# Performance work log

Measured on AMD Instinct MI355X. Metric: run time of the kernel, lower is better.

The kernel has to match this reference:

```python
import jax, jax.numpy as jnp
import numpy as np

DIM = 64; HEADS = 4; HD = DIM // HEADS; TOPK = 40; RS = 2  # region_size = max(4//t_patch,1)
B = 16; T = 2048; NR = T // RS
EPS = 1e-5
SCALE = DIM ** -0.5  # qk_scale=None -> self.dim**-0.5 (as in source, NOT head_dim)


def conv1d(x, w, pad, groups=1):
    return jax.lax.conv_general_dilated(x, w, (1,), [(pad, pad)],
        dimension_numbers=('NCH', 'OIH', 'NCH'), feature_group_count=groups)


def bn(x, g, b):
    # eval-mode BatchNorm1d with fresh running stats (mean=0, var=1)
    s = g * np.float32(1.0 / np.sqrt(1.0 + EPS))
    return x * s[None, :, None] + b[None, :, None]


def _blocks(t):
    # (B, C, T) -> (B, H, NR, RS, HD)
    return t.reshape(B, HEADS, HD, NR, RS).transpose(0, 1, 3, 4, 2)


def forward(x, n1_g, n1_b, wq, bnq_g, bnq_b, wk, bnk_g, bnk_b, wv,
            lepe_w, lepe_b, out_w, out_b, n2_g, n2_b,
            fc1_w, bn1_g, bn1_b, fr, fi, frb, fib, fc2_w, bn2_g, bn2_b):
    # ---------- Time_bra: top-k region routing attention ----------
    xn = bn(x, n1_g, n1_b)
    q = bn(conv1d(xn, wq, 1), bnq_g, bnq_b)
    k = bn(conv1d(xn, wk, 1), bnk_g, bnk_b)
    v = conv1d(xn, wv, 0)
    # region pooling on detached q/k (avg_pool1d, T divisible by RS)
    qd = jax.lax.stop_gradient(q); kd = jax.lax.stop_gradient(k)
    q_r = qd.reshape(B, DIM, NR, RS).mean(-1)
    k_r = kd.reshape(B, DIM, NR, RS).mean(-1)
    a_r = jnp.einsum('bcr,bcs->brs', q_r, k_r)          # (B, NR, NR) region affinity
    idx = jax.lax.top_k(a_r, TOPK)[1]                   # (B, NR, TOPK), shared across heads
    qb = _blocks(q); kb = _blocks(k); vb = _blocks(v)   # (B, H, NR, RS, HD)
    ie = idx[:, None, :, :, None, None]                 # (B, 1, NR, TOPK, 1, 1)
    kg = jnp.take_along_axis(kb[:, :, None], ie, axis=3).reshape(B, HEADS, NR, TOPK * RS, HD)
    vg = jnp.take_along_axis(vb[:, :, None], ie, axis=3).reshape(B, HEADS, NR, TOPK * RS, HD)
    logits = jnp.einsum('bhrqd,bhrkd->bhrqk', qb, kg) * jnp.float32(SCALE)
    attn = jax.nn.softmax(logits, axis=-1)
    o = jnp.einsum('bhrqk,bhrkd->bhrqd', attn, vg)      # (B, H, NR, RS, HD)
    o = o.transpose(0, 1, 4, 2, 3).reshape(B, DIM, T)
    o = o + conv1d(v, lepe_w, 1, groups=DIM) + lepe_b[None, :, None]  # lepe (depthwise)
    o = conv1d(o, out_w, 0) + out_b[None, :, None]
    x = x + o
    # ---------- Frequencydomain_FFN ----------
    yn = bn(x, n2_g, n2_b)
    h = jax.nn.relu(bn(conv1d(yn, fc1_w, 0), bn1_g, bn1_b))  # (B, 2C, T)
    h = h.transpose(0, 2, 1)                                  # (B, T, 2C)
    f = jnp.fft.fft(h, axis=1, norm='ortho')
    # torch.einsum('bnc,cc->bnc', x, r) contracts with diag(r) (repeated index)
    xr = jax.nn.relu(jnp.einsum('bnc,cc->bnc', f.real, fr) - jnp.einsum('bnc,cc->bnc', f.imag, fi) + frb)
    xi = jax.nn.relu(jnp.einsum('bnc,cc->bnc', f.imag, fr) + jnp.einsum('bnc,cc->bnc', f.real, fi) + fib)
    h = jnp.fft.ifft(jax.lax.complex(xr, xi), axis=1, norm='ortho').real.astype(jnp.float32)
    h = bn(conv1d(h.transpose(0, 2, 1), fc2_w, 0), bn2_g, bn2_b)
    return x + h


def setup_inputs() -> dict:
    ks = jax.random.split(jax.random.key(0), 16)
    C = DIM; C2 = 2 * DIM
    g = lambda i, shape, s: (s * jax.random.normal(ks[i], shape)).astype(jnp.float32)
    return {
        'x': jax.random.normal(ks[0], (B, C, T), dtype=jnp.float32),
        'n1_g': jnp.ones((C,), jnp.float32), 'n1_b': jnp.zeros((C,), jnp.float32),
        'wq': g(1, (C, C, 3), 0.05), 'bnq_g': jnp.ones((C,), jnp.float32), 'bnq_b': jnp.zeros((C,), jnp.float32),
        'wk': g(2, (C, C, 3), 0.05), 'bnk_g': jnp.ones((C,), jnp.float32), 'bnk_b': jnp.zeros((C,), jnp.float32),
        'wv': g(3, (C, C, 1), 0.05),
        'lepe_w': g(4, (C, 1, 3), 0.1), 'lepe_b': jnp.zeros((C,), jnp.float32),
        'out_w': g(5, (C, C, 1), 0.05), 'out_b': jnp.zeros((C,), jnp.float32),
        'n2_g': jnp.ones((C,), jnp.float32), 'n2_b': jnp.zeros((C,), jnp.float32),
        'fc1_w': g(6, (C2, C, 1), 0.05), 'bn1_g': jnp.ones((C2,), jnp.float32), 'bn1_b': jnp.zeros((C2,), jnp.float32),
        'fr': g(7, (C2, C2), 0.02), 'fi': g(8, (C2, C2), 0.02),
        'frb': g(9, (C2,), 0.02), 'fib': g(10, (C2,), 0.02),
        'fc2_w': g(11, (C, C2, 1), 0.05), 'bn2_g': jnp.ones((C,), jnp.float32), 'bn2_b': jnp.zeros((C,), jnp.float32),
    }


def reference(x, n1_g, n1_b, wq, bnq_g, bnq_b, wk, bnk_g, bnk_b, wv,
              lepe_w, lepe_b, out_w, out_b, n2_g, n2_b,
              fc1_w, bn1_g, bn1_b, fr, fi, frb, fib, fc2_w, bn2_g, bn2_b):
    return forward(x, n1_g, n1_b, wq, bnq_g, bnq_b, wk, bnk_g, bnk_b, wv,
                   lepe_w, lepe_b, out_w, out_b, n2_g, n2_b,
                   fc1_w, bn1_g, bn1_b, fr, fi, frb, fib, fc2_w, bn2_g, bn2_b)
```

## Files before the change

kernel.cpp:

```cpp
#include <hip/hip_runtime.h>
#include <hip/hip_bf16.h>

#define T 2048
#define NR 1024
#define TOPK 40

static __device__ __forceinline__ float bnscale() { return 0.9999950000374997f; }

static __device__ __forceinline__ unsigned wave_umax64(unsigned x) {
  unsigned r = x, t;
  t = (unsigned)__builtin_amdgcn_update_dpp((int)r, (int)r, 0x111, 0xf, 0xf, false); r = r > t ? r : t;
  t = (unsigned)__builtin_amdgcn_update_dpp((int)r, (int)r, 0x112, 0xf, 0xf, false); r = r > t ? r : t;
  t = (unsigned)__builtin_amdgcn_update_dpp((int)r, (int)r, 0x114, 0xf, 0xf, false); r = r > t ? r : t;
  t = (unsigned)__builtin_amdgcn_update_dpp((int)r, (int)r, 0x118, 0xf, 0xf, false); r = r > t ? r : t;
  t = (unsigned)__builtin_amdgcn_update_dpp((int)r, (int)r, 0x142, 0xf, 0xf, false); r = r > t ? r : t;
  t = (unsigned)__builtin_amdgcn_update_dpp((int)r, (int)r, 0x143, 0xf, 0xf, false); r = r > t ? r : t;
  return (unsigned)__builtin_amdgcn_readlane((int)r, 63);
}

__global__ __launch_bounds__(256) void k_qkv(
    const float* __restrict__ x, const float* __restrict__ n1_g, const float* __restrict__ n1_b,
    const float* __restrict__ wq, const float* __restrict__ bnq_g, const float* __restrict__ bnq_b,
    const float* __restrict__ wk, const float* __restrict__ bnk_g, const float* __restrict__ bnk_b,
    const float* __restrict__ wv,
    float* __restrict__ q_t, float* __restrict__ k_t, float* __restrict__ v_t,
    float* __restrict__ q_rc, float* __restrict__ k_rc)
{
  const int b = blockIdx.y;
  const int tile = blockIdx.x >> 2;
  const int oc0 = (blockIdx.x & 3) * 16;
  const int t0 = tile * 64;
  const int r0 = tile * 32;
  const int tid = threadIdx.x;
  const float INVS = bnscale();

  __shared__ float xn[64][67];
  __shared__ float ot[16][67];

  for (int i = tid; i < 64 * 66; i += 256) {
    int c = i / 66, tt = i - c * 66;
    int t = t0 + tt - 1;
    float v = (t >= 0 && t < T) ? x[(size_t)(b * 64 + c) * T + t] : 0.f;
    xn[c][tt] = v * (n1_g[c] * INVS) + n1_b[c];
  }
  __syncthreads();

  const int w = tid >> 6, lane = tid & 63;
  const int ob = oc0 + __builtin_amdgcn_readfirstlane(w) * 4;

  float accq[4], acck[4], accv[4];
#pragma unroll
  for (int j = 0; j < 4; ++j) { accq[j] = 0.f; acck[j] = 0.f; accv[j] = 0.f; }

#pragma unroll 1
  for (int c0 = 0; c0 < 64; c0 += 4) {
    float xr[4][3];
#pragma unroll
    for (int cc = 0; cc < 4; ++cc) {
      xr[cc][0] = xn[c0 + cc][lane];
      xr[cc][1] = xn[c0 + cc][lane + 1];
      xr[cc][2] = xn[c0 + cc][lane + 2];
    }
#pragma unroll
    for (int o4 = 0; o4 < 4; ++o4) {
      int o = ob + o4;
      const float* wqo = wq + o * 192 + c0 * 3;
      const float* wko = wk + o * 192 + c0 * 3;
      const float* wvo = wv + o * 64 + c0;
      float aq = accq[o4], ak = acck[o4], av = accv[o4];
#pragma unroll
      for (int cc = 0; cc < 4; ++cc) {
        aq += xr[cc][0] * wqo[cc * 3 + 0] + xr[cc][1] * wqo[cc * 3 + 1] + xr[cc][2] * wqo[cc * 3 + 2];
        ak += xr[cc][0] * wko[cc * 3 + 0] + xr[cc][1] * wko[cc * 3 + 1] + xr[cc][2] * wko[cc * 3 + 2];
        av += xr[cc][1] * wvo[cc];
      }
      accq[o4] = aq; acck[o4] = ak; accv[o4] = av;
    }
  }

#pragma unroll
  for (int o4 = 0; o4 < 4; ++o4) {
    int o = ob + o4;
    ot[o - oc0][lane] = accq[o4] * (bnq_g[o] * INVS) + bnq_b[o];
  }
  __syncthreads();
  for (int i = tid; i < 1024; i += 256) {
    int cl = i & 15, tt = i >> 4;
    q_t[((size_t)(b * T + t0 + tt)) * 64 + oc0 + cl] = ot[cl][tt];
  }
  for (int i = tid; i < 512; i += 256) {
    int rr = i & 31, cl = i >> 5;
    q_rc[((size_t)(b * 64 + oc0 + cl)) * NR + r0 + rr] = 0.5f * (ot[cl][2 * rr] + ot[cl][2 * rr + 1]);
  }
  __syncthreads();

#pragma unroll
  for (int o4 = 0; o4 < 4; ++o4) {
    int o = ob + o4;
    ot[o - oc0][lane] = acck[o4] * (bnk_g[o] * INVS) + bnk_b[o];
  }
  __syncthreads();
  for (int i = tid; i < 1024; i += 256) {
    int cl = i & 15, tt = i >> 4;
    k_t[((size_t)(b * T + t0 + tt)) * 64 + oc0 + cl] = ot[cl][tt];
  }
  for (int i = tid; i < 512; i += 256) {
    int rr = i & 31, cl = i >> 5;
    k_rc[((size_t)(b * 64 + oc0 + cl)) * NR + r0 + rr] = 0.5f * (ot[cl][2 * rr] + ot[cl][2 * rr + 1]);
  }
  __syncthreads();

#pragma unroll
  for (int o4 = 0; o4 < 4; ++o4) {
    ot[ob + o4 - oc0][lane] = accv[o4];
  }
  __syncthreads();
  for (int i = tid; i < 1024; i += 256) {
    int cl = i & 15, tt = i >> 4;
    v_t[((size_t)(b * T + t0 + tt)) * 64 + oc0 + cl] = ot[cl][tt];
  }
}

__global__ __launch_bounds__(256) void k_scores(
    const float* __restrict__ q_rc, const float* __restrict__ k_rc, int* __restrict__ sel)
{
  const int b = blockIdx.y;
  const int r0 = blockIdx.x * 16;
  const int tid = threadIdx.x;
  const int w = tid >> 6, lane = tid & 63;

  __shared__ float qsT[16][68];

  for (int i = tid; i < 1024; i += 256) {
    int rr = i & 15, c = i >> 4;
    qsT[rr][c] = q_rc[((size_t)(b * 64 + c)) * NR + r0 + rr];
  }
  __syncthreads();

  const int row0 = w * 4;

  float4 acc[4][4];
#pragma unroll
  for (int r = 0; r < 4; ++r)
#pragma unroll
    for (int j = 0; j < 4; ++j) acc[r][j] = make_float4(0.f, 0.f, 0.f, 0.f);

  const float4* kp = (const float4*)(k_rc + ((size_t)b * 64) * NR);
#pragma unroll 1
  for (int c0 = 0; c0 < 64; c0 += 4) {
    float4 qv[4];
#pragma unroll
    for (int r = 0; r < 4; ++r) qv[r] = *(const float4*)&qsT[row0 + r][c0];
#pragma unroll
    for (int cc = 0; cc < 4; ++cc) {
      const float4* kr = kp + (size_t)(c0 + cc) * 256 + lane;
      float4 k0 = kr[0], k1 = kr[64], k2 = kr[128], k3 = kr[192];
      float qf[4] = { (&qv[0].x)[cc], (&qv[1].x)[cc], (&qv[2].x)[cc], (&qv[3].x)[cc] };
#pragma unroll
      for (int r = 0; r < 4; ++r) {
        float q = qf[r];
        acc[r][0].x += q * k0.x; acc[r][0].y += q * k0.y; acc[r][0].z += q * k0.z; acc[r][0].w += q * k0.w;
        acc[r][1].x += q * k1.x; acc[r][1].y += q * k1.y; acc[r][1].z += q * k1.z; acc[r][1].w += q * k1.w;
        acc[r][2].x += q * k2.x; acc[r][2].y += q * k2.y; acc[r][2].z += q * k2.z; acc[r][2].w += q * k2.w;
        acc[r][3].x += q * k3.x; acc[r][3].y += q * k3.y; acc[r][3].z += q * k3.z; acc[r][3].w += q * k3.w;
      }
    }
  }

  unsigned pk[4][16];
#pragma unroll
  for (int r = 0; r < 4; ++r) {
#pragma unroll
    for (int j = 0; j < 4; ++j) {
      const float* av = &acc[r][j].x;
#pragma unroll
      for (int s = 0; s < 4; ++s) {
        unsigned u = __float_as_uint(av[s]);
        u ^= (unsigned)((int)u >> 31) | 0x80000000u;
        int idx = 256 * j + 4 * lane + s;
        pk[r][4 * j + s] = (u & 0xFFFFFC00u) | (unsigned)(1023 - idx);
      }
    }
#pragma unroll
    for (int k = 2; k <= 16; k <<= 1) {
#pragma unroll
      for (int j = k >> 1; j > 0; j >>= 1) {
#pragma unroll
        for (int i = 0; i < 16; ++i) {
          int l = i ^ j;
          if (l > i) {
            unsigned hi = pk[r][i] > pk[r][l] ? pk[r][i] : pk[r][l];
            unsigned lo = pk[r][i] > pk[r][l] ? pk[r][l] : pk[r][i];
            bool dir = ((i & k) == 0);
            pk[r][i] = dir ? hi : lo;
            pk[r][l] = dir ? lo : hi;
          }
        }
      }
    }
  }

  int res[4] = {0, 0, 0, 0};
#pragma unroll 1
  for (int it = 0; it < TOPK; ++it) {
#pragma unroll
    for (int r = 0; r < 4; ++r) {
      unsigned bv = wave_umax64(pk[r][0]);
      if (lane == it) res[r] = 1023 - (int)(bv & 1023u);
      bool won = (pk[r][0] == bv);
#pragma unroll
      for (int s = 0; s < 15; ++s) pk[r][s] = won ? pk[r][s + 1] : pk[r][s];
      pk[r][15] = won ? 0u : pk[r][15];
    }
  }

  if (lane < TOPK) {
#pragma unroll
    for (int r = 0; r < 4; ++r)
      sel[((size_t)(b * NR + r0 + row0 + r)) * TOPK + lane] = res[r];
  }
}

__global__ __launch_bounds__(256) void k_attn(
    const float* __restrict__ q_t, const float* __restrict__ k_t, const float* __restrict__ v_t,
    const int* __restrict__ sel, const float* __restrict__ lepe_w, const float* __restrict__ lepe_b,
    float* __restrict__ o_t)
{
  const int b = blockIdx.y;
  const int r = blockIdx.x;
  const int tid = threadIdx.x;

  __shared__ __align__(16) float kg[80][68];
  __shared__ __align__(16) float qb[2][64];
  __shared__ int   toff[80];
  __shared__ __align__(16) float lg[4][2][84];
  __shared__ float vl[4][64];

  float (*part)[2][64] = (float (*)[2][64])&kg[0][0];

  if (tid < 40) {
    int s = sel[((size_t)(b * NR + r)) * TOPK + tid];
    toff[2 * tid]     = s * 512;
    toff[2 * tid + 1] = s * 512 + 256;
  }
  if (tid >= 128 && tid < 256) {
    int i = tid - 128;
    int s = i >> 6, c = i & 63;
    qb[s][c] = q_t[((size_t)(b * T + r * 2 + s)) * 64 + c];
  }
  {
    int idx = tid >> 6, c = tid & 63;
    int t = 2 * r - 1 + idx;
    vl[idx][c] = (t >= 0 && t < T) ? v_t[((size_t)(b * T + t)) * 64 + c] : 0.f;
  }
  __syncthreads();

  {
    const char* kbase = (const char*)(k_t + (size_t)b * T * 64);
    for (int i = tid; i < 80 * 16; i += 256) {
      int row = i >> 4, c4 = i & 15;
      float4 kv = *(const float4*)(kbase + toff[row] + c4 * 16);
      *(float4*)&kg[row][c4 * 4] = kv;
    }
  }
  __syncthreads();

  const int h = tid >> 6, lane = tid & 63;

  {
    float4 q0[4], q1[4];
#pragma unroll
    for (int j = 0; j < 4; ++j) {
      q0[j] = *(const float4*)&qb[0][h * 16 + j * 4];
      q1[j] = *(const float4*)&qb[1][h * 16 + j * 4];
    }
    for (int col = lane; col < 80; col += 64) {
      float a0 = 0.f, a1 = 0.f;
#pragma unroll
      for (int j = 0; j < 4; ++j) {
        float4 kv = *(const float4*)&kg[col][h * 16 + j * 4];
        a0 += q0[j].x * kv.x + q0[j].y * kv.y + q0[j].z * kv.z + q0[j].w * kv.w;
        a1 += q1[j].x * kv.x + q1[j].y * kv.y + q1[j].z * kv.z + q1[j].w * kv.w;
      }
      lg[h][0][col] = a0 * 0.125f;
      lg[h][1][col] = a1 * 0.125f;
    }
  }

  for (int sq = 0; sq < 2; ++sq) {
    float a = lg[h][sq][lane];
    float bb = (lane < 16) ? lg[h][sq][64 + lane] : -INFINITY;
    float m = fmaxf(a, bb);
    for (int mm = 32; mm >= 1; mm >>= 1) m = fmaxf(m, __shfl_xor(m, mm));
    float ea = expf(a - m);
    float eb = (lane < 16) ? expf(bb - m) : 0.f;
    float ssum = ea + eb;
    for (int mm = 32; mm >= 1; mm >>= 1) ssum += __shfl_xor(ssum, mm);
    float inv = 1.f / ssum;
    lg[h][sq][lane] = ea * inv;
    if (lane < 16) lg[h][sq][64 + lane] = eb * inv;
  }
  __syncthreads();

  {
    const int c = tid & 63, j = tid >> 6;
    const int sq = j & 1, half = j >> 1;
    const int hh = c >> 4;
    const char* vbase = (const char*)(v_t + (size_t)b * T * 64) + c * 4;
    float acc = 0.f;
#pragma unroll 2
    for (int ch = 0; ch < 10; ++ch) {
      int col0 = half * 40 + ch * 4;
      float4 p = *(const float4*)&lg[hh][sq][col0];
      float v0 = *(const float*)(vbase + toff[col0 + 0]);
      float v1 = *(const float*)(vbase + toff[col0 + 1]);
      float v2 = *(const float*)(vbase + toff[col0 + 2]);
      float v3 = *(const float*)(vbase + toff[col0 + 3]);
      acc += p.x * v0 + p.y * v1 + p.z * v2 + p.w * v3;
    }
    part[half][sq][c] = acc;
  }
  __syncthreads();

  if (tid < 128) {
    int sq = tid >> 6, c = tid & 63;
    float o = part[0][sq][c] + part[1][sq][c];
    float lep = lepe_b[c];
#pragma unroll
    for (int kk = 0; kk < 3; ++kk) lep += lepe_w[c * 3 + kk] * vl[sq + kk][c];
    o_t[((size_t)(b * T + 2 * r + sq)) * 64 + c] = o + lep;
  }
}

__global__ __launch_bounds__(256) void k_mix(
    const float* __restrict__ x, const float* __restrict__ o_t,
    const float* __restrict__ out_w, const float* __restrict__ out_b,
    const float* __restrict__ n2_g, const float* __restrict__ n2_b,
    const float* __restrict__ fc1_w, const float* __restrict__ bn1_g, const float* __restrict__ bn1_b,
    float* __restrict__ xres, float* __restrict__ h_c)
{
  const int b = blockIdx.y;
  const int t0 = blockIdx.x * 16;
  const int tid = threadIdx.x;
  const float INVS = bnscale();

  __shared__ float ol[16][65];
  __shared__ float yn[16][65];
  __shared__ float xl[16][65];
  __shared__ float wo[64][65];
  __shared__ float w1[128][65];
  __shared__ float res2[128][17];

  for (int i = tid; i < 1024; i += 256) {
    int tt = i >> 6, c = i & 63;
    ol[tt][c] = o_t[((size_t)(b * T + t0 + tt)) * 64 + c];
  }
  for (int i = tid; i < 1024; i += 256) {
    int c = i >> 4, tt = i & 15;
    xl[tt][c] = x[(size_t)(b * 64 + c) * T + t0 + tt];
  }
  for (int i = tid; i < 4096; i += 256) {
    int c = i >> 6, cc = i & 63;
    wo[cc][c] = out_w[i];
  }
  for (int i = tid; i < 8192; i += 256) {
    int cc = i >> 6, c = i & 63;
    w1[cc][c] = fc1_w[i];
  }
  __syncthreads();

  {
    const int c = tid & 63, grp = tid >> 6;
    float a0 = out_b[c], a1 = a0, a2 = a0, a3 = a0;
    for (int cc = 0; cc < 64; ++cc) {
      float wv = wo[cc][c];
      a0 += wv * ol[grp * 4 + 0][cc];
      a1 += wv * ol[grp * 4 + 1][cc];
      a2 += wv * ol[grp * 4 + 2][cc];
      a3 += wv * ol[grp * 4 + 3][cc];
    }
    float g2 = n2_g[c] * INVS, b2 = n2_b[c];
    float av[4] = {a0, a1, a2, a3};
#pragma unroll
    for (int j = 0; j < 4; ++j) {
      int tt = grp * 4 + j;
      float xr = xl[tt][c] + av[j];
      xres[((size_t)(b * T + t0 + tt)) * 64 + c] = xr;
      yn[tt][c] = xr * g2 + b2;
    }
  }
  __syncthreads();

  {
    const int cc = tid & 127, half = tid >> 7;
    float acc[8];
#pragma unroll
    for (int j = 0; j < 8; ++j) acc[j] = 0.f;
    for (int c = 0; c < 64; ++c) {
      float wv = w1[cc][c];
#pragma unroll
      for (int j = 0; j < 8; ++j) acc[j] += wv * yn[half * 8 + j][c];
    }
    float g1 = bn1_g[cc] * INVS, b1 = bn1_b[cc];
#pragma unroll
    for (int j = 0; j < 8; ++j)
      res2[cc][half * 8 + j] = fmaxf(acc[j] * g1 + b1, 0.f);
  }
  __syncthreads();

  for (int i = tid; i < 2048; i += 256) {
    int tt = i & 15, cc = i >> 4;
    h_c[((size_t)(b * 128 + cc)) * T + t0 + tt] = res2[cc][tt];
  }
}

__global__ __launch_bounds__(256) void k_fft(
    const float* __restrict__ h_c, const float* __restrict__ fr, const float* __restrict__ fi,
    const float* __restrict__ frb, const float* __restrict__ fib, float* __restrict__ g_c)
{
  const int b = blockIdx.y;
  const int c2 = blockIdx.x;
  const int tid = threadIdx.x;

  __shared__ float re[2048];
  __shared__ float im[2048];
  __shared__ float twr[512];
  __shared__ float twi[512];

  for (int i = tid; i < 512; i += 256) {
    float ang = -6.283185307179586f * (float)i * (1.0f / 2048.0f);
    float sn, cs;
    sincosf(ang, &sn, &cs);
    twr[i] = cs; twi[i] = sn;
  }
  const float* hrow = h_c + ((size_t)(b * 128 + c2)) * T;
  for (int t = tid; t < 2048; t += 256) {
    re[t] = hrow[t];
    im[t] = 0.f;
  }
  __syncthreads();

#pragma unroll
  for (int m = 2048; m >= 8; m >>= 2) {
    const int q = m >> 2;
    const int f = 2048 / m;
#pragma unroll
    for (int k = tid; k < 512; k += 256) {
      int p = k & (q - 1);
      int g = k / q;
      int i0 = g * m + p, i1 = i0 + q, i2 = i0 + 2 * q, i3 = i0 + 3 * q;
      float a0r = re[i0], a0i = im[i0], a1r = re[i1], a1i = im[i1];
      float a2r = re[i2], a2i = im[i2], a3r = re[i3], a3i = im[i3];
      float s0r = a0r + a2r, s0i = a0i + a2i;
      float s1r = a0r - a2r, s1i = a0i - a2i;
      float s2r = a1r + a3r, s2i = a1i + a3i;
      float s3r = a1r - a3r, s3i = a1i - a3i;
      re[i0] = s0r + s2r; im[i0] = s0i + s2i;
      float y1r = s1r + s3i, y1i = s1i - s3r;
      float y2r = s0r - s2r, y2i = s0i - s2i;
      float y3r = s1r - s3i, y3i = s1i + s3r;
      float w1r = twr[f * p], w1i = twi[f * p];
      float w2r = w1r * w1r - w1i * w1i, w2i = 2.f * w1r * w1i;
      float w3r = w2r * w1r - w2i * w1i, w3i = w2r * w1i + w2i * w1r;
      re[i1] = y1r * w1r - y1i * w1i; im[i1] = y1r * w1i + y1i * w1r;
      re[i2] = y2r * w2r - y2i * w2i; im[i2] = y2r * w2i + y2i * w2r;
      re[i3] = y3r * w3r - y3i * w3i; im[i3] = y3r * w3i + y3i * w3r;
    }
    __syncthreads();
  }
  for (int k = tid; k < 1024; k += 256) {
    int i0 = 2 * k, i1 = 2 * k + 1;
    float ur = re[i0], ui = im[i0], vr = re[i1], vi = im[i1];
    re[i0] = ur + vr; im[i0] = ui + vi;
    re[i1] = ur - vr; im[i1] = ui - vi;
  }
  __syncthreads();

  const float SC = 0.022097086912079608f;
  const float fa = fr[c2 * 129];
  const float fb = fi[c2 * 129];
  const float fra = frb[c2];
  const float fia = fib[c2];
  for (int t = tid; t < 2048; t += 256) {
    float rr = re[t] * SC, ii = im[t] * SC;
    re[t] = fmaxf(rr * fa - ii * fb + fra, 0.f);
    im[t] = fmaxf(ii * fa + rr * fb + fia, 0.f);
  }
  __syncthreads();

  for (int k = tid; k < 1024; k += 256) {
    int i0 = 2 * k, i1 = 2 * k + 1;
    float ur = re[i0], ui = im[i0], vr = re[i1], vi = im[i1];
    re[i0] = ur + vr; im[i0] = ui + vi;
    re[i1] = ur - vr; im[i1] = ui - vi;
  }
  __syncthreads();
#pragma unroll
  for (int m = 8; m <= 2048; m <<= 2) {
    const int q = m >> 2;
    const int f = 2048 / m;
#pragma unroll
    for (int k = tid; k < 512; k += 256) {
      int p = k & (q - 1);
      int g = k / q;
      int i0 = g * m + p, i1 = i0 + q, i2 = i0 + 2 * q, i3 = i0 + 3 * q;
      float y0r = re[i0], y0i = im[i0];
      float b1r = re[i1], b1i = im[i1];
      float b2r = re[i2], b2i = im[i2];
      float b3r = re[i3], b3i = im[i3];
      float w1r = twr[f * p], w1i = twi[f * p];
      float w2r = w1r * w1r - w1i * w1i, w2i = 2.f * w1r * w1i;
      float w3r = w2r * w1r - w2i * w1i, w3i = w2r * w1i + w2i * w1r;
      float z1r = b1r * w1r + b1i * w1i, z1i = b1i * w1r - b1r * w1i;
      float z2r = b2r * w2r + b2i * w2i, z2i = b2i * w2r - b2r * w2i;
      float z3r = b3r * w3r + b3i * w3i, z3i = b3i * w3r - b3r * w3i;
      float u0r = y0r + z2r, u0i = y0i + z2i;
      float u2r = y0r - z2r, u2i = y0i - z2i;
      float u1r = z1r + z3r, u1i = z1i + z3i;
      float dr = z1r - z3r, di = z1i - z3i;
      float u3r = -di, u3i = dr;
      re[i0] = u0r + u1r; im[i0] = u0i + u1i;
      re[i2] = u0r - u1r; im[i2] = u0i - u1i;
      re[i1] = u2r + u3r; im[i1] = u2i + u3i;
      re[i3] = u2r - u3r; im[i3] = u2i - u3i;
    }
    __syncthreads();
  }

  float* grow = g_c + ((size_t)(b * 128 + c2)) * T;
  for (int t = tid; t < 2048; t += 256)
    grow[t] = re[t] * SC;
}

__global__ __launch_bounds__(256) void k_out(
    const float* __restrict__ g_c, const float* __restrict__ xres,
    const float* __restrict__ fc2_w, const float* __restrict__ bn2_g, const float* __restrict__ bn2_b,
    float* __restrict__ out)
{
  const int b = blockIdx.y;
  const int t0 = blockIdx.x * 16;
  const int tid = threadIdx.x;
  const float INVS = bnscale();

  __shared__ float gl[16][129];
  __shared__ float w2[128][65];
  __shared__ float res[64][17];

  for (int i = tid; i < 2048; i += 256) {
    int tt = i & 15, cc = i >> 4;
    gl[tt][cc] = g_c[((size_t)(b * 128 + cc)) * T + t0 + tt];
  }
  for (int i = tid; i < 8192; i += 256) {
    int c = i >> 7, cc = i & 127;
    w2[cc][c] = fc2_w[i];
  }
  __syncthreads();

  {
    const int c = tid & 63, grp = tid >> 6;
    float a0 = 0.f, a1 = 0.f, a2 = 0.f, a3 = 0.f;
    for (int cc = 0; cc < 128; ++cc) {
      float wv = w2[cc][c];
      a0 += wv * gl[grp * 4 + 0][cc];
      a1 += wv * gl[grp * 4 + 1][cc];
      a2 += wv * gl[grp * 4 + 2][cc];
      a3 += wv * gl[grp * 4 + 3][cc];
    }
    float g2 = bn2_g[c] * INVS, b2 = bn2_b[c];
    float av[4] = {a0, a1, a2, a3};
#pragma unroll
    for (int j = 0; j < 4; ++j) {
      int tt = grp * 4 + j;
      res[c][tt] = xres[((size_t)(b * T + t0 + tt)) * 64 + c] + av[j] * g2 + b2;
    }
  }
  __syncthreads();

  for (int i = tid; i < 1024; i += 256) {
    int tt = i & 15, c = i >> 4;
    out[(size_t)(b * 64 + c) * T + t0 + tt] = res[c][tt];
  }
}

extern "C" void kernel_launch(void* const* d_in, const int* in_sizes, int n_in,
                              void* d_out, int out_size, void* d_ws, size_t ws_size,
                              hipStream_t stream) {
  (void)in_sizes; (void)n_in; (void)out_size; (void)ws_size;
  const float* x     = (const float*)d_in[0];
  const float* n1_g  = (const float*)d_in[1];
  const float* n1_b  = (const float*)d_in[2];
  const float* wq    = (const float*)d_in[3];
  const float* bnq_g = (const float*)d_in[4];
  const float* bnq_b = (const float*)d_in[5];
  const float* wk    = (const float*)d_in[6];
  const float* bnk_g = (const float*)d_in[7];
  const float* bnk_b = (const float*)d_in[8];
  const float* wv    = (const float*)d_in[9];
  const float* lepe_w= (const float*)d_in[10];
  const float* lepe_b= (const float*)d_in[11];
  const float* out_w = (const float*)d_in[12];
  const float* out_b = (const float*)d_in[13];
  const float* n2_g  = (const float*)d_in[14];
  const float* n2_b  = (const float*)d_in[15];
  const float* fc1_w = (const float*)d_in[16];
  const float* bn1_g = (const float*)d_in[17];
  const float* bn1_b = (const float*)d_in[18];
  const float* fr    = (const float*)d_in[19];
  const float* fi    = (const float*)d_in[20];
  const float* frb   = (const float*)d_in[21];
  const float* fib   = (const float*)d_in[22];
  const float* fc2_w = (const float*)d_in[23];
  const float* bn2_g = (const float*)d_in[24];
  const float* bn2_b = (const float*)d_in[25];

  float* out = (float*)d_out;
  float* ws  = (float*)d_ws;
  const size_t M1 = (size_t)1 << 20;

  float* q_t  = ws;
  float* k_t  = ws + 2 * M1;
  float* v_t  = ws + 4 * M1;
  float* q_rc = ws + 6 * M1;
  float* k_rc = ws + 7 * M1;
  float* o_t  = ws + 8 * M1;
  float* xrs  = ws + 10 * M1;
  int*   sel  = (int*)(ws + 12 * M1);
  float* h_c  = ws;
  float* g_c  = ws + 4 * M1;

  k_qkv<<<dim3(128, 16), 256, 0, stream>>>(x, n1_g, n1_b, wq, bnq_g, bnq_b,
                                           wk, bnk_g, bnk_b, wv, q_t, k_t, v_t, q_rc, k_rc);
  k_scores<<<dim3(64, 16), 256, 0, stream>>>(q_rc, k_rc, sel);
  k_attn<<<dim3(1024, 16), 256, 0, stream>>>(q_t, k_t, v_t, sel, lepe_w, lepe_b, o_t);
  k_mix<<<dim3(128, 16), 256, 0, stream>>>(x, o_t, out_w, out_b, n2_g, n2_b,
                                           fc1_w, bn1_g, bn1_b, xrs, h_c);
  k_fft<<<dim3(128, 16), 256, 0, stream>>>(h_c, fr, fi, frb, fib, g_c);
  k_out<<<dim3(128, 16), 256, 0, stream>>>(g_c, xrs, fc2_w, bn2_g, bn2_b, out);
}
```

Baseline: 426.8 us.

## Replace bitonic sort top-k with radix threshold search using ballots

Replaces the per-lane bitonic sort and the 40 rounds of wave-wide max extraction with a bitwise radix search for the top-k threshold, counting candidates via ballot/popcount. Selected indices are then written through ballot-based compaction. This removes the sort network and the repeated DPP reductions and register shifts, at the cost of up to 32 passes of 16 ballots per row. The output order of selected indices changes from sorted-by-score to lane/position order.

```diff
diff --git a/kernel.cpp b/kernel.cpp
--- a/kernel.cpp
+++ b/kernel.cpp
@@ -6,17 +6,6 @@
 #define TOPK 40
 
 static __device__ __forceinline__ float bnscale() { return 0.9999950000374997f; }
-
-static __device__ __forceinline__ unsigned wave_umax64(unsigned x) {
-  unsigned r = x, t;
-  t = (unsigned)__builtin_amdgcn_update_dpp((int)r, (int)r, 0x111, 0xf, 0xf, false); r = r > t ? r : t;
-  t = (unsigned)__builtin_amdgcn_update_dpp((int)r, (int)r, 0x112, 0xf, 0xf, false); r = r > t ? r : t;
-  t = (unsigned)__builtin_amdgcn_update_dpp((int)r, (int)r, 0x114, 0xf, 0xf, false); r = r > t ? r : t;
-  t = (unsigned)__builtin_amdgcn_update_dpp((int)r, (int)r, 0x118, 0xf, 0xf, false); r = r > t ? r : t;
-  t = (unsigned)__builtin_amdgcn_update_dpp((int)r, (int)r, 0x142, 0xf, 0xf, false); r = r > t ? r : t;
-  t = (unsigned)__builtin_amdgcn_update_dpp((int)r, (int)r, 0x143, 0xf, 0xf, false); r = r > t ? r : t;
-  return (unsigned)__builtin_amdgcn_readlane((int)r, 63);
-}
 
 __global__ __launch_bounds__(256) void k_qkv(
     const float* __restrict__ x, const float* __restrict__ n1_g, const float* __restrict__ n1_b,
@@ -181,43 +170,44 @@
         pk[r][4 * j + s] = (u & 0xFFFFFC00u) | (unsigned)(1023 - idx);
       }
     }
-#pragma unroll
-    for (int k = 2; k <= 16; k <<= 1) {
-#pragma unroll
-      for (int j = k >> 1; j > 0; j >>= 1) {
-#pragma unroll
-        for (int i = 0; i < 16; ++i) {
-          int l = i ^ j;
-          if (l > i) {
-            unsigned hi = pk[r][i] > pk[r][l] ? pk[r][i] : pk[r][l];
-            unsigned lo = pk[r][i] > pk[r][l] ? pk[r][l] : pk[r][i];
-            bool dir = ((i & k) == 0);
-            pk[r][i] = dir ? hi : lo;
-            pk[r][l] = dir ? lo : hi;
-          }
-        }
-      }
-    }
-  }
-
-  int res[4] = {0, 0, 0, 0};
+  }
+
+  unsigned p[4] = {0u, 0u, 0u, 0u};
+  unsigned thr[4];
+  bool done[4] = {false, false, false, false};
 #pragma unroll 1
-  for (int it = 0; it < TOPK; ++it) {
+  for (int bit = 31; bit >= 0; --bit) {
 #pragma unroll
     for (int r = 0; r < 4; ++r) {
-      unsigned bv = wave_umax64(pk[r][0]);
-      if (lane == it) res[r] = 1023 - (int)(bv & 1023u);
-      bool won = (pk[r][0] == bv);
-#pragma unroll
-      for (int s = 0; s < 15; ++s) pk[r][s] = won ? pk[r][s + 1] : pk[r][s];
-      pk[r][15] = won ? 0u : pk[r][15];
-    }
-  }
-
-  if (lane < TOPK) {
-#pragma unroll
-    for (int r = 0; r < 4; ++r)
-      sel[((size_t)(b * NR + r0 + row0 + r)) * TOPK + lane] = res[r];
+      if (done[r]) continue;
+      unsigned X = p[r] | (1u << bit);
+      int c = 0;
+#pragma unroll
+      for (int j = 0; j < 16; ++j)
+        c += __popcll(__ballot(pk[r][j] >= X));
+      if (c >= TOPK) p[r] = X;
+      if (c == TOPK) { thr[r] = X; done[r] = true; }
+    }
+    if (done[0] && done[1] && done[2] && done[3]) break;
+  }
+#pragma unroll
+  for (int r = 0; r < 4; ++r)
+    if (!done[r]) thr[r] = p[r];
+
+#pragma unroll
+  for (int r = 0; r < 4; ++r) {
+    const unsigned X = thr[r];
+    int* srow = sel + ((size_t)(b * NR + r0 + row0 + r)) * TOPK;
+    int base = 0;
+#pragma unroll
+    for (int j = 0; j < 16; ++j) {
+      bool win = pk[r][j] >= X;
+      unsigned long long m = __ballot(win);
+      int before = __builtin_amdgcn_mbcnt_hi((unsigned)(m >> 32),
+                   __builtin_amdgcn_mbcnt_lo((unsigned)m, 0));
+      if (win) srow[base + before] = 1023 - (int)(pk[r][j] & 1023u);
+      base += __popcll(m);
+    }
   }
 }
 
```

Result: no change. 433.8 us (+1.6%).
